# Kernel tuning notes

Measured on AMD Instinct MI355X. Metric: run time of the kernel, lower is better.

Reference implementation:

```python
import jax, jax.numpy as jnp
import numpy as np

B, N, M = 8, 1024, 64          # graphs, ops/graph, machines/graph
OPF, MF = 16, 8                # raw feature dims
H, D, L = 8, 64, 3             # heads, head dim, HGT layers
F = H * D                      # 512 = hidden_dim * num_heads
KC = 8                         # compatible machines per op
NOP, NM = B * N, B * M
EPS = 1e-5


def _graph_ln(x, w, b):
    # PyG LayerNorm(mode='graph') with batch=None: scalar mean/std over the whole tensor
    x = x - x.mean()
    return x / (x.std() + EPS) * w + b


def _seg_softmax(a, idx, n):
    amax = jax.ops.segment_max(a, idx, num_segments=n)
    amax = jnp.where(jnp.isfinite(amax), amax, 0.0)
    ex = jnp.exp(a - amax[idx])
    s = jax.ops.segment_sum(ex, idx, num_segments=n)
    return ex / (s[idx] + 1e-16)


def _forward(op_x, machine_x, W_emb_op, b_emb_op, W_emb_m, b_emb_m,
             opn_w, opn_b, mn_w, mn_b, Wk, bk, Wq, bq, Wv, bv,
             A_rel, M_rel, p_rel, W_out, b_out, skip, ln_w, ln_b,
             ei_precedes, ei_canproc, ei_compat):
    x_op = _graph_ln(op_x @ W_emb_op + b_emb_op, opn_w, opn_b)
    x_m = _graph_ln(machine_x @ W_emb_m + b_emb_m, mn_w, mn_b)
    s0, d0 = ei_precedes   # op -> op
    s1, d1 = ei_canproc    # machine -> op
    s2, d2 = ei_compat     # op -> machine
    scale = 1.0 / jnp.sqrt(jnp.float32(D))
    for l in range(L):
        k_op = (x_op @ Wk[l, 0] + bk[l, 0]).reshape(NOP, H, D)
        q_op = (x_op @ Wq[l, 0] + bq[l, 0]).reshape(NOP, H, D)
        v_op = (x_op @ Wv[l, 0] + bv[l, 0]).reshape(NOP, H, D)
        k_m = (x_m @ Wk[l, 1] + bk[l, 1]).reshape(NM, H, D)
        q_m = (x_m @ Wq[l, 1] + bq[l, 1]).reshape(NM, H, D)
        v_m = (x_m @ Wv[l, 1] + bv[l, 1]).reshape(NM, H, D)
        # relation-specific per-head transforms (a_rel/m_rel of HGTConv)
        k0 = jnp.einsum('nhd,hde->nhe', k_op, A_rel[l, 0]); v0 = jnp.einsum('nhd,hde->nhe', v_op, M_rel[l, 0])
        k1 = jnp.einsum('nhd,hde->nhe', k_m, A_rel[l, 1]);  v1 = jnp.einsum('nhd,hde->nhe', v_m, M_rel[l, 1])
        k2 = jnp.einsum('nhd,hde->nhe', k_op, A_rel[l, 2]); v2 = jnp.einsum('nhd,hde->nhe', v_op, M_rel[l, 2])
        # attention into op nodes: joint softmax over both incoming edge types
        a0 = (q_op[d0] * k0[s0]).sum(-1) * p_rel[l, 0] * scale   # [E0,H]
        a1 = (q_op[d1] * k1[s1]).sum(-1) * p_rel[l, 1] * scale   # [E1,H]
        a_op = jnp.concatenate([a0, a1]); dd = jnp.concatenate([d0, d1])
        w = _seg_softmax(a_op, dd, NOP)
        msg = jnp.concatenate([v0[s0], v1[s1]]) * w[:, :, None]
        agg_op = jax.ops.segment_sum(msg, dd, num_segments=NOP).reshape(NOP, F)
        # attention into machine nodes
        a2 = (q_m[d2] * k2[s2]).sum(-1) * p_rel[l, 2] * scale
        w2 = _seg_softmax(a2, d2, NM)
        agg_m = jax.ops.segment_sum(v2[s2] * w2[:, :, None], d2, num_segments=NM).reshape(NM, F)
        # output projection + learned skip gate (HGTConv internals)
        o_op = jax.nn.gelu(agg_op, approximate=False) @ W_out[l, 0] + b_out[l, 0]
        o_m = jax.nn.gelu(agg_m, approximate=False) @ W_out[l, 1] + b_out[l, 1]
        g_op = jax.nn.sigmoid(skip[l, 0]); g_m = jax.nn.sigmoid(skip[l, 1])
        o_op = g_op * o_op + (1.0 - g_op) * x_op
        o_m = g_m * o_m + (1.0 - g_m) * x_m
        # wrapper residual + dropout(eval=identity) + graph layer norm
        x_op = _graph_ln(o_op + x_op, ln_w[l], ln_b[l])
        x_m = _graph_ln(o_m + x_m, ln_w[l], ln_b[l])
    fea_j = x_op.reshape(B, N, F)
    fea_m = x_m.reshape(B, M, F)
    return fea_j, fea_m, fea_j.mean(1, keepdims=True), fea_m.mean(1, keepdims=True)


def setup_inputs() -> dict:
    key = jax.random.key(0)
    ks = jax.random.split(key, 12)
    rng = np.random.default_rng(0)
    ids = np.arange(NOP).reshape(B, N)
    src0 = ids[:, :-1].ravel(); dst0 = ids[:, 1:].ravel()
    mach = rng.integers(0, M, size=(B, N, KC)) + (np.arange(B) * M)[:, None, None]
    ops = np.broadcast_to(ids[:, :, None], (B, N, KC))
    ei_precedes = jnp.asarray(np.stack([src0, dst0]), dtype=jnp.int32)
    ei_canproc = jnp.asarray(np.stack([mach.ravel(), ops.ravel()]), dtype=jnp.int32)
    ei_compat = jnp.asarray(np.stack([ops.ravel(), mach.ravel()]), dtype=jnp.int32)
    n = lambda k, sh, s=0.05: jax.random.normal(k, sh, dtype=jnp.float32) * s
    return dict(
        op_x=n(ks[0], (NOP, OPF), 1.0),
        machine_x=n(ks[1], (NM, MF), 1.0),
        W_emb_op=n(ks[2], (OPF, F)), b_emb_op=jnp.zeros((F,), jnp.float32),
        W_emb_m=n(ks[3], (MF, F)), b_emb_m=jnp.zeros((F,), jnp.float32),
        opn_w=jnp.ones((F,), jnp.float32), opn_b=jnp.zeros((F,), jnp.float32),
        mn_w=jnp.ones((F,), jnp.float32), mn_b=jnp.zeros((F,), jnp.float32),
        Wk=n(ks[4], (L, 2, F, F)), bk=jnp.zeros((L, 2, F), jnp.float32),
        Wq=n(ks[5], (L, 2, F, F)), bq=jnp.zeros((L, 2, F), jnp.float32),
        Wv=n(ks[6], (L, 2, F, F)), bv=jnp.zeros((L, 2, F), jnp.float32),
        A_rel=n(ks[7], (L, 3, H, D, D)), M_rel=n(ks[8], (L, 3, H, D, D)),
        p_rel=jnp.ones((L, 3, H), jnp.float32),
        W_out=n(ks[9], (L, 2, F, F)), b_out=jnp.zeros((L, 2, F), jnp.float32),
        skip=jnp.ones((L, 2), jnp.float32),
        ln_w=jnp.ones((L, F), jnp.float32), ln_b=jnp.zeros((L, F), jnp.float32),
        ei_precedes=ei_precedes, ei_canproc=ei_canproc, ei_compat=ei_compat,
    )


def reference(op_x, machine_x, W_emb_op, b_emb_op, W_emb_m, b_emb_m,
              opn_w, opn_b, mn_w, mn_b, Wk, bk, Wq, bq, Wv, bv,
              A_rel, M_rel, p_rel, W_out, b_out, skip, ln_w, ln_b,
              ei_precedes, ei_canproc, ei_compat):
    return _forward(op_x, machine_x, W_emb_op, b_emb_op, W_emb_m, b_emb_m,
                    opn_w, opn_b, mn_w, mn_b, Wk, bk, Wq, bq, Wv, bv,
                    A_rel, M_rel, p_rel, W_out, b_out, skip, ln_w, ln_b,
                    ei_precedes, ei_canproc, ei_compat)
```

## Files before the change

kernel.cpp:

```cpp
#include <hip/hip_runtime.h>

typedef unsigned short u16;
typedef __attribute__((ext_vector_type(4))) float floatx4;
typedef __attribute__((ext_vector_type(8))) short shortx8;
typedef __attribute__((ext_vector_type(4))) short shortx4;

#define NOPS 8192
#define NMS  512
#define CQ   2560
#define CM   1536
#define NE2  65536
#define TOPC (NOPS*512)
#define TMC  (NMS*512)

__device__ __forceinline__ float bf2f(u16 u){ return __uint_as_float(((unsigned)u)<<16); }
__device__ __forceinline__ u16 f2bf(float f){
  unsigned u = __float_as_uint(f);
  u += 0x7FFFu + ((u>>16)&1u);
  return (u16)(u>>16);
}
__device__ __forceinline__ float wred(float v){
  #pragma unroll
  for (int o=32;o;o>>=1) v += __shfl_xor(v,o,64);
  return v;
}
__device__ __forceinline__ float wredmax(float v){
  #pragma unroll
  for (int o=32;o;o>>=1) v = fmaxf(v, __shfl_xor(v,o,64));
  return v;
}
__device__ __forceinline__ float geluf(float x){
  return 0.5f*x*(1.f+erff(x*0.70710678118654752f));
}
__device__ __forceinline__ void block_stat_out2(float s, float s2, float* pstat, int slot){
  __shared__ float sb[8];
  s = wred(s); s2 = wred(s2);
  int wv = threadIdx.x >> 6;
  if ((threadIdx.x & 63) == 0){ sb[wv*2] = s; sb[wv*2+1] = s2; }
  __syncthreads();
  if (threadIdx.x == 0){
    float a = 0.f, b = 0.f;
    int nw = blockDim.x >> 6;
    for (int i=0;i<nw;++i){ a += sb[i*2]; b += sb[i*2+1]; }
    pstat[slot*2]   = a;
    pstat[slot*2+1] = b;
  }
}

__global__ __launch_bounds__(256) void cnt2_k(const int* __restrict__ s1, float* __restrict__ Ct,
                                              float* __restrict__ Cn){
  int idx = blockIdx.x*256 + threadIdx.x;
  int n = idx >> 6, l = idx & 63;
  const int* row = s1 + n*8;
  int cnt = 0;
  #pragma unroll
  for (int j=0;j<8;++j) cnt += ((row[j] & 63) == l);
  float f = (float)cnt;
  Cn[(size_t)n*64 + l] = f;
  int b = n >> 10, nl = n & 1023;
  Ct[(size_t)((b<<6) + l)*1024 + nl] = f;
}

__global__ __launch_bounds__(256) void twout_k(const float* __restrict__ src, u16* __restrict__ dst){
  __shared__ u16 t[64][65];
  int l = blockIdx.x, kb = blockIdx.y*64, nb = blockIdx.z*64;
  const float* s = src + (size_t)l*262144;
  u16* d = dst + (size_t)l*262144;
  int tx = threadIdx.x & 63, ty4 = threadIdx.x >> 6;
  #pragma unroll 4
  for (int p=0;p<16;++p){
    int k = ty4 + p*4;
    t[k][tx] = f2bf(s[(size_t)(kb+k)*512 + nb + tx]);
  }
  __syncthreads();
  #pragma unroll 4
  for (int p=0;p<16;++p){
    int n = ty4 + p*4;
    d[(size_t)(nb+n)*512 + kb + tx] = t[tx][n];
  }
}

__global__ __launch_bounds__(256) void tq_k(const float* __restrict__ Wq,
                                            u16* __restrict__ Wc_op_t, u16* __restrict__ Wc_m_t){
  __shared__ u16 tl[64][65];
  int blk = blockIdx.x;
  int l = blk >> 1, side = blk & 1;
  const float* s = Wq + (size_t)blk*262144;
  u16* d = side ? (Wc_m_t + (size_t)l*CM*512) : (Wc_op_t + (size_t)l*CQ*512);
  int kb = blockIdx.y*64, nb = blockIdx.z*64;
  int tx = threadIdx.x & 63, ty4 = threadIdx.x >> 6;
  #pragma unroll 4
  for (int p=0;p<16;++p){
    int k = ty4 + p*4;
    tl[k][tx] = f2bf(s[(size_t)(kb+k)*512 + nb + tx]);
  }
  __syncthreads();
  #pragma unroll 4
  for (int p=0;p<16;++p){
    int n = ty4 + p*4;
    d[(size_t)(nb+n)*512 + kb + tx] = tl[tx][n];
  }
}

__global__ void qb_k(const float* __restrict__ bq, float* bias_op, float* bias_m){
  int i = blockIdx.x*blockDim.x + threadIdx.x;
  if (i >= 3072) return;
  int l = i >> 10, side = (i >> 9) & 1, f = i & 511;
  float v = bq[(l*2+side)*512 + f];
  if (side==0) bias_op[l*CQ + f] = v; else bias_m[l*CM + f] = v;
}

__global__ __launch_bounds__(256) void combine3_k(const float* __restrict__ Wk, const float* __restrict__ Wv,
                                                  const float* __restrict__ Ar, const float* __restrict__ Mr,
                                                  u16* __restrict__ Wc_op_t, u16* __restrict__ Wc_m_t){
  __shared__ u16 As[64*72];
  __shared__ u16 Bs[128*72];
  int gx = blockIdx.x;
  int l = gx/48; int rem = gx - l*48; int s = rem >> 3; int h = rem & 7;
  int side = (s < 4) ? 0 : 1;
  int r = (s < 4) ? (s+1) : (s-3);
  int useK = side==0 ? (s==0 || s==2) : (s==4);
  int rel  = side==0 ? ((s<2)?0:2) : 1;
  const float* W   = (useK ? Wk : Wv) + (size_t)(l*2+side)*262144;
  const float* Rel = (useK ? Ar : Mr) + ((size_t)(l*3+rel)*8 + h)*4096;
  int h64 = h*64;
  u16* Wt = side ? (Wc_m_t + (size_t)l*CM*512) : (Wc_op_t + (size_t)l*CQ*512);
  int rbase = r*512 + h64;
  int cc0 = blockIdx.y * 128;
  int tid = threadIdx.x, lane = tid & 63, wave = tid >> 6;
  {
    int d = tid >> 2, e0 = (tid & 3) * 16;
    #pragma unroll
    for (int j=0;j<16;++j) As[(e0+j)*72 + d] = f2bf(Rel[d*64 + e0 + j]);
  }
  {
    int ccl = tid >> 1, d0 = (tid & 1) * 32;
    const float* src = W + (size_t)(cc0+ccl)*512 + h64 + d0;
    #pragma unroll
    for (int j=0;j<32;j+=4){
      floatx4 v = *(const floatx4*)(src + j);
      shortx4 sv;
      #pragma unroll
      for (int e=0;e<4;++e) sv[e] = (short)f2bf(v[e]);
      *(shortx4*)(Bs + ccl*72 + d0 + j) = sv;
    }
  }
  __syncthreads();
  int wm = wave & 1, wn = wave >> 1;
  int mrow = lane & 15, quad = lane >> 4;
  floatx4 acc[2][4];
  #pragma unroll
  for (int a=0;a<2;++a)
    #pragma unroll
    for (int b=0;b<4;++b) acc[a][b] = (floatx4){0.f,0.f,0.f,0.f};
  #pragma unroll
  for (int ks=0; ks<2; ++ks){
    shortx8 af[2], bf[4];
    #pragma unroll
    for (int mt=0;mt<2;++mt) af[mt] = *(const shortx8*)(As + (wm*32 + mt*16 + mrow)*72 + ks*32 + quad*8);
    #pragma unroll
    for (int nt=0;nt<4;++nt) bf[nt] = *(const shortx8*)(Bs + (wn*64 + nt*16 + mrow)*72 + ks*32 + quad*8);
    #pragma unroll
    for (int mt=0;mt<2;++mt)
      #pragma unroll
      for (int nt=0;nt<4;++nt)
        acc[mt][nt] = __builtin_amdgcn_mfma_f32_16x16x32_bf16(af[mt], bf[nt], acc[mt][nt], 0, 0, 0);
  }
  #pragma unroll
  for (int mt=0;mt<2;++mt){
    #pragma unroll
    for (int nt=0;nt<4;++nt){
      int ccl = wn*64 + nt*16 + mrow;
      #pragma unroll
      for (int r2=0;r2<4;++r2){
        int e = wm*32 + mt*16 + quad*4 + r2;
        Wt[(size_t)(rbase + e)*512 + cc0 + ccl] = f2bf(acc[mt][nt][r2]);
      }
    }
  }
}
__global__ void cbias_k(const float* __restrict__ bk, const float* __restrict__ bv,
                        const float* __restrict__ Ar, const float* __restrict__ Mr,
                        float* bias_op, float* bias_m){
  int gx = blockIdx.x; int e = threadIdx.x;
  int l = gx/48; int rem = gx - l*48; int s = rem >> 3; int h = rem & 7;
  int side = (s < 4) ? 0 : 1;
  int r = (s < 4) ? (s+1) : (s-3);
  int useK = side==0 ? (s==0 || s==2) : (s==4);
  int rel  = side==0 ? ((s<2)?0:2) : 1;
  const float* bb  = (useK ? bk : bv) + (size_t)(l*2+side)*512 + h*64;
  const float* Rel = (useK ? Ar : Mr) + ((size_t)(l*3+rel)*8 + h)*4096;
  float acc = 0.f;
  for (int d=0; d<64; ++d) acc += bb[d]*Rel[d*64 + e];
  float* bias = side ? (bias_m + l*CM) : (bias_op + l*CQ);
  bias[r*512 + h*64 + e] = acc;
}

__global__ __launch_bounds__(256) void embed2_k(const float* __restrict__ Xop, const float* __restrict__ Wop,
                                                const float* __restrict__ bop, float* __restrict__ Yop,
                                                const float* __restrict__ Xm, const float* __restrict__ Wm,
                                                const float* __restrict__ bm_, float* __restrict__ Ym,
                                                float* pstat, float* pstat_m){
  int bid = blockIdx.x;
  const float *X, *W, *bias; float *Y, *ps; int K, total, nb, lb;
  if (bid < 1024){ X=Xop; W=Wop; bias=bop; Y=Yop; ps=pstat;   K=16; total=TOPC; nb=1024; lb=bid; }
  else           { X=Xm;  W=Wm;  bias=bm_; Y=Ym;  ps=pstat_m; K=8;  total=TMC;  nb=128;  lb=bid-1024; }
  float s = 0.f, s2 = 0.f;
  for (int idx = lb*256 + threadIdx.x; idx < total; idx += nb*256){
    int n = idx >> 9, f = idx & 511;
    float v = bias[f];
    for (int c=0;c<K;++c) v += X[n*K+c] * W[c*512+f];
    Y[idx] = v;
    s += v; s2 += v*v;
  }
  block_stat_out2(s, s2, ps, lb);
}

__global__ __launch_bounds__(256) void ln2_k(const float* __restrict__ src_op, float* __restrict__ dst_op,
                                             u16* __restrict__ dbf_op, const float* __restrict__ w_op,
                                             const float* __restrict__ b_op,
                                             const float* __restrict__ src_m, float* __restrict__ dst_m,
                                             u16* __restrict__ dbf_m, const float* __restrict__ w_m,
                                             const float* __restrict__ b_m,
                                             const float* __restrict__ pstat, const float* __restrict__ pstat_m,
                                             int nbo, int nbm){
  int bid = blockIdx.x;
  const float *src, *w, *b, *ps; float* dst; u16* dbf; int total4, nb, lb, nblk; float inv_n;
  if (bid < 1024){ src=src_op; dst=dst_op; dbf=dbf_op; w=w_op; b=b_op; ps=pstat;
                   total4=TOPC/4; nb=1024; lb=bid; nblk=nbo; inv_n=1.f/TOPC; }
  else           { src=src_m;  dst=dst_m;  dbf=dbf_m;  w=w_m;  b=b_m;  ps=pstat_m;
                   total4=TMC/4;  nb=128;  lb=bid-1024; nblk=nbm; inv_n=1.f/TMC; }
  __shared__ float sb[8];
  __shared__ float mr[2];
  float s = 0.f, s2 = 0.f;
  for (int i = threadIdx.x; i < nblk; i += 256){ s += ps[2*i]; s2 += ps[2*i+1]; }
  s = wred(s); s2 = wred(s2);
  int wv = threadIdx.x >> 6;
  if ((threadIdx.x & 63) == 0){ sb[wv*2] = s; sb[wv*2+1] = s2; }
  __syncthreads();
  if (threadIdx.x == 0){
    float a = 0.f, bsum = 0.f;
    for (int i=0;i<4;++i){ a += sb[i*2]; bsum += sb[i*2+1]; }
    float mean = a * inv_n;
    float var  = fmaxf(bsum * inv_n - mean*mean, 0.f);
    mr[0] = mean;
    mr[1] = 1.f/(sqrtf(var) + 1e-5f);
  }
  __syncthreads();
  float mean = mr[0], rinv = mr[1];
  const floatx4* s4 = (const floatx4*)src;
  floatx4* d4 = (floatx4*)dst;
  shortx4* db4 = (shortx4*)dbf;
  const floatx4* w4 = (const floatx4*)w;
  const floatx4* b4 = (const floatx4*)b;
  for (int i = lb*256 + threadIdx.x; i < total4; i += nb*256){
    int f = i & 127;
    floatx4 v = s4[i], wv2 = w4[f], bv = b4[f];
    shortx4 sv;
    #pragma unroll
    for (int e=0;e<4;++e){ v[e] = (v[e]-mean)*rinv*wv2[e] + bv[e]; sv[e] = (short)f2bf(v[e]); }
    d4[i] = v;
    db4[i] = sv;
  }
}

__device__ __forceinline__ void gemm_gate_core(u16* As, u16* Bs, const u16* __restrict__ A,
                                               const u16* __restrict__ Bt,
                                               const float* __restrict__ xr, const float* __restrict__ bo,
                                               const float* __restrict__ sk, float* __restrict__ Y,
                                               float* pstat, int slot, int bx, int by){
  const int tid = threadIdx.x;
  const int lane = tid & 63, wave = tid >> 6;
  const int bm = by * 128, bn = bx * 128;
  const int wm = wave & 1, wn = wave >> 1;
  const int mrow = lane & 15, quad = lane >> 4;
  const u16* Ab = A + (size_t)bm*512;
  const u16* Bb = Bt + (size_t)bn*512;
  floatx4 acc[4][4];
  #pragma unroll
  for (int a=0;a<4;++a)
    #pragma unroll
    for (int b=0;b<4;++b) acc[a][b] = (floatx4){0.f,0.f,0.f,0.f};
  const int r0 = tid >> 2, c0 = (tid & 3) * 8;
  const int r1 = (tid+256) >> 2, c1 = ((tid+256) & 3) * 8;
  const int lds0 = wave*512;
  const int lds1 = wave*512 + 2048;
  for (int k0 = 0; k0 < 512; k0 += 32){
    __builtin_amdgcn_global_load_lds((const __attribute__((address_space(1))) void*)(Ab + (size_t)r0*512 + k0 + c0),
                                     (__attribute__((address_space(3))) void*)(As + lds0), 16, 0, 0);
    __builtin_amdgcn_global_load_lds((const __attribute__((address_space(1))) void*)(Ab + (size_t)r1*512 + k0 + c1),
                                     (__attribute__((address_space(3))) void*)(As + lds1), 16, 0, 0);
    __builtin_amdgcn_global_load_lds((const __attribute__((address_space(1))) void*)(Bb + (size_t)r0*512 + k0 + c0),
                                     (__attribute__((address_space(3))) void*)(Bs + lds0), 16, 0, 0);
    __builtin_amdgcn_global_load_lds((const __attribute__((address_space(1))) void*)(Bb + (size_t)r1*512 + k0 + c1),
                                     (__attribute__((address_space(3))) void*)(Bs + lds1), 16, 0, 0);
    __syncthreads();
    shortx8 af[4], bf[4];
    #pragma unroll
    for (int mt=0;mt<4;++mt) af[mt] = *(const shortx8*)(As + (wm*64 + mt*16 + mrow)*32 + quad*8);
    #pragma unroll
    for (int nt=0;nt<4;++nt) bf[nt] = *(const shortx8*)(Bs + (wn*64 + nt*16 + mrow)*32 + quad*8);
    #pragma unroll
    for (int mt=0;mt<4;++mt)
      #pragma unroll
      for (int nt=0;nt<4;++nt)
        acc[mt][nt] = __builtin_amdgcn_mfma_f32_16x16x32_bf16(af[mt], bf[nt], acc[mt][nt], 0, 0, 0);
    __syncthreads();
  }
  float g = 1.f/(1.f+expf(-(*sk)));
  float s = 0.f, s2 = 0.f;
  #pragma unroll
  for (int mt=0;mt<4;++mt){
    #pragma unroll
    for (int nt=0;nt<4;++nt){
      int col = bn + wn*64 + nt*16 + mrow;
      float bval = bo[col];
      #pragma unroll
      for (int r2=0;r2<4;++r2){
        int row = bm + wm*64 + mt*16 + quad*4 + r2;
        float v = acc[mt][nt][r2] + bval;
        float o = g*v + (2.f-g)*xr[(size_t)row*512 + col];
        Y[(size_t)row*512 + col] = o;
        s += o; s2 += o*o;
      }
    }
  }
  block_stat_out2(s, s2, pstat, slot);
}
__global__ __launch_bounds__(256) void gemmgate2_k(const u16* A1, const u16* B1, const float* x1,
                                                   const float* bo1, const float* sk1, float* Y1, float* ps1,
                                                   int nblk1,
                                                   const u16* A2, const u16* B2, const float* x2,
                                                   const float* bo2, const float* sk2, float* Y2, float* ps2){
  __shared__ u16 As[128*32];
  __shared__ u16 Bs[128*32];
  int id = blockIdx.x;
  if (id < nblk1) gemm_gate_core(As, Bs, A1, B1, x1, bo1, sk1, Y1, ps1, id, id % 4, id / 4);
  else { int j = id - nblk1; gemm_gate_core(As, Bs, A2, B2, x2, bo2, sk2, Y2, ps2, j, j % 4, j / 4); }
}

__device__ __forceinline__ void stage_half8(const u16* __restrict__ src, int kc, u16* region, int tid){
  int wave = tid >> 6;
  #pragma unroll
  for (int j=0;j<2;++j){
    int idx = j*512 + tid;
    int row = idx >> 2, qp2 = idx & 3;
    int qs = qp2 ^ (((row >> 3) & 1) << 1);
    __builtin_amdgcn_global_load_lds(
      (const __attribute__((address_space(1))) void*)(src + (size_t)row*512 + kc + qs*8),
      (__attribute__((address_space(3))) void*)(region + (j*512 + wave*64)*8),
      16, 0, 0);
  }
}

#define MFMA_QUAD(MH) do { \
  __builtin_amdgcn_s_barrier(); \
  asm volatile("s_waitcnt lgkmcnt(0)" ::: "memory"); \
  __builtin_amdgcn_sched_barrier(0); \
  __builtin_amdgcn_s_setprio(1); \
  _Pragma("unroll") \
  for (int mt=0;mt<4;++mt){ \
    _Pragma("unroll") \
    for (int nt=0;nt<4;++nt) \
      acc[(MH)*4+mt][nt] = __builtin_amdgcn_mfma_f32_16x16x32_bf16(af[mt], bf[nt], acc[(MH)*4+mt][nt], 0, 0, 0); \
  } \
  __builtin_amdgcn_s_setprio(0); \
} while(0)

__global__ __launch_bounds__(512, 2) void gemm8_k(
    const u16* __restrict__ A1, const u16* __restrict__ B1, const float* __restrict__ bias1,
    u16* __restrict__ C1, int N1, int nbx1, int nblk1,
    const u16* __restrict__ A2, const u16* __restrict__ B2, const float* __restrict__ bias2,
    u16* __restrict__ C2, int N2, int nbx2){
  extern __shared__ u16 lds[];
  int id = blockIdx.x;
  const u16 *A, *Bt; const float* bias; u16* C; int N, bx, by;
  if (id < nblk1){
    int xcd = id & 7, loc = id >> 3;
    int wg = xcd * (nblk1 >> 3) + loc;
    A=A1; Bt=B1; bias=bias1; C=C1; N=N1; bx=wg%nbx1; by=wg/nbx1;
  }
  else { int j=id-nblk1; A=A2; Bt=B2; bias=bias2; C=C2; N=N2; bx=j%nbx2; by=j/nbx2; }
  const int tid = threadIdx.x, lane = tid & 63, wave = tid >> 6;
  const int wm = wave & 1, wn = wave >> 1;
  const int mrow = lane & 15, quad = lane >> 4;
  const int qp = quad ^ ((mrow & 8) ? 2 : 0);
  const u16* Ab = A + (size_t)(by*256)*512;
  const u16* Bb = Bt + (size_t)(bx*256)*512;

  floatx4 acc[8][4];
  #pragma unroll
  for (int a=0;a<8;++a)
    #pragma unroll
    for (int b=0;b<4;++b) acc[a][b] = (floatx4){0.f,0.f,0.f,0.f};

  stage_half8(Ab, 0,  lds,          tid);
  stage_half8(Bb, 0,  lds + 16384,  tid);
  stage_half8(Ab, 32, lds + 8192,   tid);
  stage_half8(Bb, 32, lds + 24576,  tid);
  stage_half8(Ab, 64, lds + 32768,  tid);
  stage_half8(Bb, 64, lds + 49152,  tid);
  asm volatile("s_waitcnt vmcnt(8)" ::: "memory");
  __builtin_amdgcn_s_barrier();

  for (int t = 0; t < 8; ++t){
    const int s = t & 1;
    u16* Sbase = lds + s*32768;
    u16* Obase = lds + (s^1)*32768;
    const u16* a0 = Sbase + (wm*128 + mrow)*32 + qp*8;
    const u16* b0 = Sbase + 16384 + (wn*64 + mrow)*32 + qp*8;
    const int kc1 = ((t < 7) ? (t+1) : 7)*64 + 32;
    const int kc2 = ((t < 6) ? (t+2) : 7)*64;
    shortx8 af[4], bf[4];

    #pragma unroll
    for (int mt=0;mt<4;++mt) af[mt] = *(const shortx8*)(a0 + mt*512);
    #pragma unroll
    for (int nt=0;nt<4;++nt) bf[nt] = *(const shortx8*)(b0 + nt*512);
    stage_half8(Ab, kc1, Obase + 8192, tid);
    MFMA_QUAD(0);
    __builtin_amdgcn_s_barrier();

    #pragma unroll
    for (int mt=0;mt<4;++mt) af[mt] = *(const shortx8*)(a0 + 2048 + mt*512);
    stage_half8(Bb, kc1, Obase + 24576, tid);
    MFMA_QUAD(1);
    asm volatile("s_waitcnt vmcnt(8)" ::: "memory");
    __builtin_amdgcn_s_barrier();

    #pragma unroll
    for (int mt=0;mt<4;++mt) af[mt] = *(const shortx8*)(a0 + 8192 + mt*512);
    #pragma unroll
    for (int nt=0;nt<4;++nt) bf[nt] = *(const shortx8*)(b0 + 8192 + nt*512);
    stage_half8(Ab, kc2, Sbase, tid);
    MFMA_QUAD(0);
    __builtin_amdgcn_s_barrier();

    #pragma unroll
    for (int mt=0;mt<4;++mt) af[mt] = *(const shortx8*)(a0 + 8192 + 2048 + mt*512);
    stage_half8(Bb, kc2, Sbase + 16384, tid);
    MFMA_QUAD(1);
    asm volatile("s_waitcnt vmcnt(8)" ::: "memory");
    __builtin_amdgcn_s_barrier();
  }

  const int crow0 = by*256 + wm*128 + quad*4;
  const int ccol0 = bx*256 + wn*64 + mrow;
  float bv[4];
  #pragma unroll
  for (int nt=0;nt<4;++nt) bv[nt] = bias ? bias[ccol0 + nt*16] : 0.f;
  #pragma unroll
  for (int mh=0;mh<2;++mh){
    #pragma unroll
    for (int mt=0;mt<4;++mt){
      int row = crow0 + mh*64 + mt*16;
      #pragma unroll
      for (int nt=0;nt<4;++nt){
        int col = ccol0 + nt*16;
        #pragma unroll
        for (int r2=0;r2<4;++r2)
          C[(size_t)(row+r2)*N + col] = f2bf(acc[mh*4+mt][nt][r2] + bv[nt]);
      }
    }
  }
}

__global__ __launch_bounds__(256) void qk12_k(const u16* __restrict__ qkv_op, const u16* __restrict__ qkv_m,
                                              const float* __restrict__ prel, const float* __restrict__ Cn,
                                              u16* __restrict__ W1, float* __restrict__ wpre,
                                              float* __restrict__ linv, float* __restrict__ S2f){
  __shared__ __align__(16) char smem[36864];
  u16* As = (u16*)smem;
  u16* Bs = As + 128*72;
  float* Sbuf = (float*)smem;
  int bh = blockIdx.y; int b = bh >> 3, h = bh & 7;
  int n0 = blockIdx.x * 128;
  int tid = threadIdx.x, lane = tid & 63, wave = tid >> 6;
  int mrow = lane & 15, quad = lane >> 4;
  if (blockIdx.z == 0){
    int wm = wave & 1, wn = wave >> 1;
    float p1 = prel[8 + h] * 0.125f;
    {
      int row = tid >> 1, col = (tid & 1) * 32;
      const u16* src = qkv_op + (size_t)(b*1024 + n0 + row)*CQ + h*64 + col;
      #pragma unroll
      for (int e=0;e<4;++e) *(shortx8*)(As + row*72 + col + e*8) = *(const shortx8*)(src + e*8);
    }
    {
      int row = tid >> 2, col = (tid & 3) * 16;
      const u16* src = qkv_m + (size_t)(b*64 + row)*CM + 512 + h*64 + col;
      *(shortx8*)(Bs + row*72 + col)     = *(const shortx8*)(src);
      *(shortx8*)(Bs + row*72 + col + 8) = *(const shortx8*)(src + 8);
    }
    __syncthreads();
    floatx4 acc[4][2];
    #pragma unroll
    for (int a=0;a<4;++a){ acc[a][0] = (floatx4){0,0,0,0}; acc[a][1] = (floatx4){0,0,0,0}; }
    #pragma unroll
    for (int ks=0; ks<2; ++ks){
      shortx8 af[4], bf[2];
      #pragma unroll
      for (int mt=0;mt<4;++mt) af[mt] = *(const shortx8*)(As + (wm*64 + mt*16 + mrow)*72 + ks*32 + quad*8);
      #pragma unroll
      for (int nt=0;nt<2;++nt) bf[nt] = *(const shortx8*)(Bs + (wn*32 + nt*16 + mrow)*72 + ks*32 + quad*8);
      #pragma unroll
      for (int mt=0;mt<4;++mt)
        #pragma unroll
        for (int nt=0;nt<2;++nt)
          acc[mt][nt] = __builtin_amdgcn_mfma_f32_16x16x32_bf16(af[mt], bf[nt], acc[mt][nt], 0, 0, 0);
    }
    __syncthreads();
    #pragma unroll
    for (int mt=0;mt<4;++mt){
      #pragma unroll
      for (int nt=0;nt<2;++nt){
        int m = wn*32 + nt*16 + mrow;
        #pragma unroll
        for (int r2=0;r2<4;++r2){
          int nl = wm*64 + mt*16 + quad*4 + r2;
          Sbuf[nl*65 + m] = acc[mt][nt][r2] * p1;
        }
      }
    }
    __syncthreads();
    if (tid < 128){
      int n_g = b*1024 + n0 + tid;
      int nl  = n0 + tid;
      float sp = -1e30f;
      if (nl > 0){
        float p0 = prel[h] * 0.125f;
        const u16* qp = qkv_op + (size_t)n_g*CQ + h*64;
        const u16* kp = qkv_op + (size_t)(n_g-1)*CQ + 512 + h*64;
        float d = 0.f;
        #pragma unroll
        for (int j=0;j<8;++j){
          shortx8 qa = *(const shortx8*)(qp + j*8);
          shortx8 ka = *(const shortx8*)(kp + j*8);
          #pragma unroll
          for (int e=0;e<8;++e) d += bf2f((u16)qa[e])*bf2f((u16)ka[e]);
        }
        sp = d * p0;
      }
      const float* crow = Cn + (size_t)n_g*64;
      float mx = sp;
      #pragma unroll
      for (int m=0;m<64;++m){
        if (crow[m] > 0.f) mx = fmaxf(mx, Sbuf[tid*65 + m]);
      }
      float L = 0.f;
      u16* wrow = W1 + ((size_t)n_g*8 + h)*64;
      #pragma unroll
      for (int m0=0;m0<64;m0+=4){
        shortx4 pv;
        #pragma unroll
        for (int e=0;e<4;++e){
          float c = crow[m0+e];
          float w = (c > 0.f) ? c*expf(Sbuf[tid*65 + m0+e]-mx) : 0.f;
          L += w;
          pv[e] = (short)f2bf(w);
        }
        *(shortx4*)(wrow + m0) = pv;
      }
      float ep = (nl > 0) ? expf(sp - mx) : 0.f;
      L += ep;
      wpre[(size_t)n_g*8 + h] = ep;
      linv[(size_t)n_g*8 + h] = 1.f/(L + 1e-16f);
    }
  } else {
    float p2 = prel[16 + h] * 0.125f;
    {
      int row = tid >> 2, col = (tid & 3) * 16;
      const u16* src = qkv_m + (size_t)(b*64+row)*CM + h*64 + col;
      *(shortx8*)(As + row*72 + col)     = *(const shortx8*)(src);
      *(shortx8*)(As + row*72 + col + 8) = *(const shortx8*)(src + 8);
    }
    {
      int row = tid >> 1, col = (tid & 1) * 32;
      const u16* src = qkv_op + (size_t)(b*1024 + n0 + row)*CQ + 1536 + h*64 + col;
      #pragma unroll
      for (int e=0;e<4;++e) *(shortx8*)(Bs + row*72 + col + e*8) = *(const shortx8*)(src + e*8);
    }
    __syncthreads();
    floatx4 acc[4][2];
    #pragma unroll
    for (int a=0;a<4;++a){ acc[a][0] = (floatx4){0,0,0,0}; acc[a][1] = (floatx4){0,0,0,0}; }
    #pragma unroll
    for (int ks=0; ks<2; ++ks){
      shortx8 af[4], bf[2];
      #pragma unroll
      for (int mt=0;mt<4;++mt) af[mt] = *(const shortx8*)(As + (mt*16 + mrow)*72 + ks*32 + quad*8);
      #pragma unroll
      for (int nt=0;nt<2;++nt) bf[nt] = *(const shortx8*)(Bs + (wave*32 + nt*16 + mrow)*72 + ks*32 + quad*8);
      #pragma unroll
      for (int mt=0;mt<4;++mt)
        #pragma unroll
        for (int nt=0;nt<2;++nt)
          acc[mt][nt] = __builtin_amdgcn_mfma_f32_16x16x32_bf16(af[mt], bf[nt], acc[mt][nt], 0, 0, 0);
    }
    #pragma unroll
    for (int mt=0;mt<4;++mt){
      #pragma unroll
      for (int nt=0;nt<2;++nt){
        int n = n0 + wave*32 + nt*16 + mrow;
        #pragma unroll
        for (int r2=0;r2<4;++r2){
          int m = mt*16 + quad*4 + r2;
          S2f[((size_t)(b*64 + m)*8 + h)*1024 + n] = acc[mt][nt][r2] * p2;
        }
      }
    }
  }
}

__global__ __launch_bounds__(512) void msoftm_k(const float* __restrict__ S2f, const float* __restrict__ Ct,
                                                u16* __restrict__ W2){
  int m = blockIdx.x;
  int h = threadIdx.x >> 6, d = threadIdx.x & 63;
  const float* srow = S2f + ((size_t)m*8 + h)*1024;
  const float* crow = Ct + (size_t)m*1024;
  float s[16], c[16];
  #pragma unroll
  for (int it=0; it<16; ++it){ s[it] = srow[it*64 + d]; c[it] = crow[it*64 + d]; }
  float mx = -1e30f;
  #pragma unroll
  for (int it=0; it<16; ++it) if (c[it] > 0.f) mx = fmaxf(mx, s[it]);
  mx = wredmax(mx);
  float e[16], L = 0.f;
  #pragma unroll
  for (int it=0; it<16; ++it){
    e[it] = (c[it] > 0.f) ? c[it]*expf(s[it]-mx) : 0.f;
    L += e[it];
  }
  L = wred(L);
  float inv = 1.f/(L + 1e-16f);
  u16* wrow = W2 + ((size_t)m*8 + h)*1024;
  #pragma unroll
  for (int it=0; it<16; ++it) wrow[it*64 + d] = f2bf(e[it]*inv);
}

__global__ __launch_bounds__(256) void agg12_k(const u16* __restrict__ W1, const u16* __restrict__ qkv_op,
                                               const u16* __restrict__ qkv_m, const float* __restrict__ wpre,
                                               const float* __restrict__ linv, u16* __restrict__ agg_op,
                                               const u16* __restrict__ W2, u16* __restrict__ agg_m){
  __shared__ u16 As[128*72];
  __shared__ u16 Bs[64*72];
  int bid = blockIdx.x;
  int tid = threadIdx.x, lane = tid & 63, wave = tid >> 6;
  int wm = wave & 1, wn = wave >> 1;
  int mrow = lane & 15, quad = lane >> 4;
  if (bid < 512){
    int bh = bid >> 3; int b = bh >> 3, h = bh & 7;
    int n0 = (bid & 7) * 128;
    {
      int row = tid >> 1, col = (tid & 1) * 32;
      const u16* src = W1 + ((size_t)(b*1024 + n0 + row)*8 + h)*64 + col;
      #pragma unroll
      for (int e=0;e<4;++e) *(shortx8*)(As + row*72 + col + e*8) = *(const shortx8*)(src + e*8);
    }
    {
      int m = tid >> 2, dcol = (tid & 3) * 16;
      const u16* src = qkv_m + (size_t)(b*64 + m)*CM + 1024 + h*64 + dcol;
      shortx8 v0 = *(const shortx8*)(src);
      shortx8 v1 = *(const shortx8*)(src + 8);
      #pragma unroll
      for (int e=0;e<8;++e){ Bs[(dcol+e)*72 + m] = (u16)v0[e]; Bs[(dcol+8+e)*72 + m] = (u16)v1[e]; }
    }
    __syncthreads();
    floatx4 acc[4][2];
    #pragma unroll
    for (int a=0;a<4;++a){ acc[a][0] = (floatx4){0,0,0,0}; acc[a][1] = (floatx4){0,0,0,0}; }
    #pragma unroll
    for (int ks=0; ks<2; ++ks){
      shortx8 af[4], bf[2];
      #pragma unroll
      for (int mt=0;mt<4;++mt) af[mt] = *(const shortx8*)(As + (wm*64 + mt*16 + mrow)*72 + ks*32 + quad*8);
      #pragma unroll
      for (int nt=0;nt<2;++nt) bf[nt] = *(const shortx8*)(Bs + (wn*32 + nt*16 + mrow)*72 + ks*32 + quad*8);
      #pragma unroll
      for (int mt=0;mt<4;++mt)
        #pragma unroll
        for (int nt=0;nt<2;++nt)
          acc[mt][nt] = __builtin_amdgcn_mfma_f32_16x16x32_bf16(af[mt], bf[nt], acc[mt][nt], 0, 0, 0);
    }
    #pragma unroll
    for (int mt=0;mt<4;++mt){
      #pragma unroll
      for (int nt=0;nt<2;++nt){
        int d = wn*32 + nt*16 + mrow;
        #pragma unroll
        for (int r2=0;r2<4;++r2){
          int n = n0 + wm*64 + mt*16 + quad*4 + r2;
          size_t ng = (size_t)b*1024 + n;
          size_t ih = ng*8 + h;
          float v = acc[mt][nt][r2];
          if ((n & 1023) > 0) v += wpre[ih] * bf2f(qkv_op[(ng-1)*CQ + 1024 + h*64 + d]);
          v *= linv[ih];
          agg_op[ng*512 + h*64 + d] = f2bf(geluf(v));
        }
      }
    }
  } else {
    int bh = bid - 512; int b = bh >> 3, h = bh & 7;
    floatx4 acc[2][2];
    acc[0][0]=(floatx4){0,0,0,0}; acc[0][1]=(floatx4){0,0,0,0};
    acc[1][0]=(floatx4){0,0,0,0}; acc[1][1]=(floatx4){0,0,0,0};
    const int arow = tid >> 2, acol = (tid & 3) * 8;
    const int nrow = tid >> 3, dcol = (tid & 7) * 8;
    for (int ks = 0; ks < 32; ++ks){
      int nn0 = ks*32;
      *(shortx8*)(As + arow*40 + acol) =
          *(const shortx8*)(W2 + ((size_t)(b*64 + arow)*8 + h)*1024 + nn0 + acol);
      shortx8 vv = *(const shortx8*)(qkv_op + (size_t)(b*1024 + nn0 + nrow)*CQ + 2048 + h*64 + dcol);
      #pragma unroll
      for (int e=0;e<8;++e) Bs[(dcol+e)*40 + nrow] = (u16)vv[e];
      __syncthreads();
      shortx8 af[2], bf[2];
      #pragma unroll
      for (int mt=0;mt<2;++mt) af[mt] = *(const shortx8*)(As + (wm*32 + mt*16 + mrow)*40 + quad*8);
      #pragma unroll
      for (int nt=0;nt<2;++nt) bf[nt] = *(const shortx8*)(Bs + (wn*32 + nt*16 + mrow)*40 + quad*8);
      #pragma unroll
      for (int mt=0;mt<2;++mt)
        #pragma unroll
        for (int nt=0;nt<2;++nt)
          acc[mt][nt] = __builtin_amdgcn_mfma_f32_16x16x32_bf16(af[mt], bf[nt], acc[mt][nt], 0, 0, 0);
      __syncthreads();
    }
    #pragma unroll
    for (int mt=0;mt<2;++mt){
      #pragma unroll
      for (int nt=0;nt<2;++nt){
        int dd = wn*32 + nt*16 + mrow;
        #pragma unroll
        for (int r2=0;r2<4;++r2){
          int m = wm*32 + mt*16 + quad*4 + r2;
          agg_m[(size_t)(b*64 + m)*512 + h*64 + dd] = f2bf(geluf(acc[mt][nt][r2]));
        }
      }
    }
  }
}

__global__ __launch_bounds__(512) void meanj_part_k(const float* __restrict__ xo, float* scratchJ){
  int b = blockIdx.x, chunk = blockIdx.y, f = threadIdx.x;
  float s = 0.f;
  for (int r=0;r<128;++r){
    int row = b*1024 + chunk*128 + r;
    s += xo[(size_t)row*512 + f];
  }
  scratchJ[(b*8 + chunk)*512 + f] = s;
}
__global__ __launch_bounds__(512) void mean2_k(const float* __restrict__ scratchJ, float* __restrict__ out){
  int i = blockIdx.x*512 + threadIdx.x;
  if (i < 4096){
    int b = i >> 9, f = i & 511;
    float s = 0.f;
    #pragma unroll
    for (int c=0;c<8;++c) s += scratchJ[(b*8+c)*512 + f];
    out[4456448 + i] = s * (1.f/1024.f);
  } else {
    int j = i - 4096;
    int b = j >> 9, f = j & 511;
    float s = 0.f;
    for (int r=0;r<64;++r) s += out[(size_t)TOPC + (size_t)(b*64+r)*512 + f];
    out[4460544 + j] = s * (1.f/64.f);
  }
}

extern "C" void kernel_launch(void* const* d_in, const int* in_sizes, int n_in,
                              void* d_out, int out_size, void* d_ws, size_t ws_size,
                              hipStream_t stream){
  const float* op_x      = (const float*)d_in[0];
  const float* machine_x = (const float*)d_in[1];
  const float* W_emb_op  = (const float*)d_in[2];
  const float* b_emb_op  = (const float*)d_in[3];
  const float* W_emb_m   = (const float*)d_in[4];
  const float* b_emb_m   = (const float*)d_in[5];
  const float* opn_w     = (const float*)d_in[6];
  const float* opn_b     = (const float*)d_in[7];
  const float* mn_w      = (const float*)d_in[8];
  const float* mn_b      = (const float*)d_in[9];
  const float* Wk        = (const float*)d_in[10];
  const float* bk        = (const float*)d_in[11];
  const float* Wq        = (const float*)d_in[12];
  const float* bq        = (const float*)d_in[13];
  const float* Wv        = (const float*)d_in[14];
  const float* bv        = (const float*)d_in[15];
  const float* A_rel     = (const float*)d_in[16];
  const float* M_rel     = (const float*)d_in[17];
  const float* p_rel     = (const float*)d_in[18];
  const float* W_out     = (const float*)d_in[19];
  const float* b_out     = (const float*)d_in[20];
  const float* skip      = (const float*)d_in[21];
  const float* ln_w      = (const float*)d_in[22];
  const float* ln_b      = (const float*)d_in[23];
  const int* s1          = (const int*)d_in[25];
  float* out = (float*)d_out;

  char* ws = (char*)d_ws;
  size_t off = 0;
  auto alloc = [&](size_t bytes)->void*{
    void* p = ws + off;
    off = (off + bytes + 255) & ~(size_t)255;
    return p;
  };
  float* pstat     = (float*)alloc(4096*4);
  float* scratchJ  = (float*)alloc(32768*4);
  float* Ct        = (float*)alloc((size_t)NMS*1024*4);
  float* Cn        = (float*)alloc((size_t)NOPS*64*4);
  float* S2f       = (float*)alloc((size_t)NMS*8*1024*4);
  u16*   W2        = (u16*)  alloc((size_t)NMS*8*1024*2);
  u16*   W1        = (u16*)  alloc((size_t)NOPS*8*64*2);
  float* wpre      = (float*)alloc((size_t)NOPS*8*4);
  float* linv      = (float*)alloc((size_t)NOPS*8*4);
  float* x_op      = (float*)alloc((size_t)NOPS*512*4);
  u16*   x_op_bf   = (u16*)  alloc((size_t)NOPS*512*2);
  float* x_m       = (float*)alloc((size_t)NMS*512*4);
  u16*   x_m_bf    = (u16*)  alloc((size_t)NMS*512*2);
  u16*   qkv_op    = (u16*)  alloc((size_t)NOPS*CQ*2);
  u16*   qkv_m     = (u16*)  alloc((size_t)NMS*CM*2);
  u16*   agg_op    = (u16*)  alloc((size_t)NOPS*512*2);
  u16*   agg_m     = (u16*)  alloc((size_t)NMS*512*2);
  u16*   Wc_op_t   = (u16*)  alloc((size_t)3*CQ*512*2);
  float* bias_op   = (float*)alloc((size_t)3*CQ*4);
  u16*   Wc_m_t    = (u16*)  alloc((size_t)3*CM*512*2);
  float* bias_m    = (float*)alloc((size_t)3*CM*4);
  u16*   Wout_t    = (u16*)  alloc((size_t)6*262144*2);
  float* o_op      = (float*)qkv_op;
  float* o_m       = (float*)qkv_m;
  float* pstat_m   = pstat + 2048;

  cnt2_k<<<2048,256,0,stream>>>(s1, Ct, Cn);
  twout_k<<<dim3(6,8,8),256,0,stream>>>(W_out, Wout_t);
  tq_k<<<dim3(6,8,8),256,0,stream>>>(Wq, Wc_op_t, Wc_m_t);
  qb_k<<<12,256,0,stream>>>(bq, bias_op, bias_m);
  combine3_k<<<dim3(144,4),256,0,stream>>>(Wk, Wv, A_rel, M_rel, Wc_op_t, Wc_m_t);
  cbias_k<<<144,64,0,stream>>>(bk, bv, A_rel, M_rel, bias_op, bias_m);

  embed2_k<<<1152,256,0,stream>>>(op_x, W_emb_op, b_emb_op, x_op,
                                  machine_x, W_emb_m, b_emb_m, x_m, pstat, pstat_m);
  ln2_k<<<1152,256,0,stream>>>(x_op, x_op, x_op_bf, opn_w, opn_b,
                               x_m, x_m, x_m_bf, mn_w, mn_b, pstat, pstat_m, 1024, 128);

  for (int l=0; l<3; ++l){
    int last = (l == 2);
    gemm8_k<<<332,512,131072,stream>>>(x_op_bf, Wc_op_t + (size_t)l*CQ*512, bias_op + l*CQ, qkv_op, CQ, 10, 320,
                                       x_m_bf, Wc_m_t + (size_t)l*CM*512, bias_m + l*CM, qkv_m, CM, 6);
    qk12_k<<<dim3(8,64,2),256,0,stream>>>(qkv_op, qkv_m, p_rel + l*24, Cn, W1, wpre, linv, S2f);
    msoftm_k<<<NMS,512,0,stream>>>(S2f, Ct, W2);
    agg12_k<<<576,256,0,stream>>>(W1, qkv_op, qkv_m, wpre, linv, agg_op, W2, agg_m);
    gemmgate2_k<<<272,256,0,stream>>>(agg_op, Wout_t + (size_t)(l*2+0)*262144, x_op,
                                      b_out + (size_t)(l*2+0)*512, skip + l*2+0, o_op, pstat, 256,
                                      agg_m, Wout_t + (size_t)(l*2+1)*262144, x_m,
                                      b_out + (size_t)(l*2+1)*512, skip + l*2+1, o_m, pstat_m);
    ln2_k<<<1152,256,0,stream>>>(o_op, last ? out : x_op, x_op_bf, ln_w + l*512, ln_b + l*512,
                                 o_m, last ? (out + TOPC) : x_m, x_m_bf, ln_w + l*512, ln_b + l*512,
                                 pstat, pstat_m, 256, 16);
  }

  meanj_part_k<<<dim3(8,8),512,0,stream>>>(out, scratchJ);
  mean2_k<<<16,512,0,stream>>>(scratchJ, out);
}
```

Before: 615.5 us.

## Fuse op-side attention aggregation into qk12 kernel and merge weight transposes

The op-node attention aggregation (P·V1 MFMA plus the predecessor term, normalisation and GELU) now runs inside qk12_k. The softmax weights, pre-edge weight and inverse sum stay in shared memory instead of being written to global W1/wpre/linv and read back by a separate kernel. The machine-side aggregation becomes its own small kernel of 64 blocks, and the two weight transpose kernels merge into one launch. This removes global round trips and launches, but qk12_k now needs 64KB of LDS, which may lower occupancy.

```diff
diff --git a/kernel.cpp b/kernel.cpp
--- a/kernel.cpp
+++ b/kernel.cpp
@@ -61,11 +61,21 @@
   Ct[(size_t)((b<<6) + l)*1024 + nl] = f;
 }
 
-__global__ __launch_bounds__(256) void twout_k(const float* __restrict__ src, u16* __restrict__ dst){
+__global__ __launch_bounds__(256) void tw_k(const float* __restrict__ Wout, const float* __restrict__ Wq,
+                                            u16* __restrict__ Wout_t, u16* __restrict__ Wc_op_t,
+                                            u16* __restrict__ Wc_m_t){
   __shared__ u16 t[64][65];
-  int l = blockIdx.x, kb = blockIdx.y*64, nb = blockIdx.z*64;
-  const float* s = src + (size_t)l*262144;
-  u16* d = dst + (size_t)l*262144;
+  int g = blockIdx.x;
+  const float* s; u16* d;
+  if (g < 6){
+    s = Wout + (size_t)g*262144;
+    d = Wout_t + (size_t)g*262144;
+  } else {
+    int blk = g - 6; int l = blk >> 1, side = blk & 1;
+    s = Wq + (size_t)blk*262144;
+    d = side ? (Wc_m_t + (size_t)l*CM*512) : (Wc_op_t + (size_t)l*CQ*512);
+  }
+  int kb = blockIdx.y*64, nb = blockIdx.z*64;
   int tx = threadIdx.x & 63, ty4 = threadIdx.x >> 6;
   #pragma unroll 4
   for (int p=0;p<16;++p){
@@ -77,28 +87,6 @@
   for (int p=0;p<16;++p){
     int n = ty4 + p*4;
     d[(size_t)(nb+n)*512 + kb + tx] = t[tx][n];
-  }
-}
-
-__global__ __launch_bounds__(256) void tq_k(const float* __restrict__ Wq,
-                                            u16* __restrict__ Wc_op_t, u16* __restrict__ Wc_m_t){
-  __shared__ u16 tl[64][65];
-  int blk = blockIdx.x;
-  int l = blk >> 1, side = blk & 1;
-  const float* s = Wq + (size_t)blk*262144;
-  u16* d = side ? (Wc_m_t + (size_t)l*CM*512) : (Wc_op_t + (size_t)l*CQ*512);
-  int kb = blockIdx.y*64, nb = blockIdx.z*64;
-  int tx = threadIdx.x & 63, ty4 = threadIdx.x >> 6;
-  #pragma unroll 4
-  for (int p=0;p<16;++p){
-    int k = ty4 + p*4;
-    tl[k][tx] = f2bf(s[(size_t)(kb+k)*512 + nb + tx]);
-  }
-  __syncthreads();
-  #pragma unroll 4
-  for (int p=0;p<16;++p){
-    int n = ty4 + p*4;
-    d[(size_t)(nb+n)*512 + kb + tx] = tl[tx][n];
   }
 }
 
@@ -467,12 +455,15 @@
 
 __global__ __launch_bounds__(256) void qk12_k(const u16* __restrict__ qkv_op, const u16* __restrict__ qkv_m,
                                               const float* __restrict__ prel, const float* __restrict__ Cn,
-                                              u16* __restrict__ W1, float* __restrict__ wpre,
-                                              float* __restrict__ linv, float* __restrict__ S2f){
-  __shared__ __align__(16) char smem[36864];
+                                              float* __restrict__ S2f, u16* __restrict__ agg_op){
+  __shared__ __align__(16) char smem[65536];
   u16* As = (u16*)smem;
   u16* Bs = As + 128*72;
   float* Sbuf = (float*)smem;
+  u16* P     = (u16*)(smem + 36864);
+  u16* v1T   = (u16*)(smem + 55296);
+  float* linvS = (float*)(smem + 64512);
+  float* wpreS = (float*)(smem + 65024);
   int bh = blockIdx.y; int b = bh >> 3, h = bh & 7;
   int n0 = blockIdx.x * 128;
   int tid = threadIdx.x, lane = tid & 63, wave = tid >> 6;
@@ -491,6 +482,14 @@
       const u16* src = qkv_m + (size_t)(b*64 + row)*CM + 512 + h*64 + col;
       *(shortx8*)(Bs + row*72 + col)     = *(const shortx8*)(src);
       *(shortx8*)(Bs + row*72 + col + 8) = *(const shortx8*)(src + 8);
+    }
+    {
+      int m = tid >> 2, dcol = (tid & 3) * 16;
+      const u16* src = qkv_m + (size_t)(b*64 + m)*CM + 1024 + h*64 + dcol;
+      shortx8 v0 = *(const shortx8*)(src);
+      shortx8 v1 = *(const shortx8*)(src + 8);
+      #pragma unroll
+      for (int e=0;e<8;++e){ v1T[(dcol+e)*72 + m] = (u16)v0[e]; v1T[(dcol+8+e)*72 + m] = (u16)v1[e]; }
     }
     __syncthreads();
     floatx4 acc[4][2];
@@ -548,7 +547,7 @@
         if (crow[m] > 0.f) mx = fmaxf(mx, Sbuf[tid*65 + m]);
       }
       float L = 0.f;
-      u16* wrow = W1 + ((size_t)n_g*8 + h)*64;
+      u16* prow = P + tid*72;
       #pragma unroll
       for (int m0=0;m0<64;m0+=4){
         shortx4 pv;
@@ -559,12 +558,46 @@
           L += w;
           pv[e] = (short)f2bf(w);
         }
-        *(shortx4*)(wrow + m0) = pv;
+        *(shortx4*)(prow + m0) = pv;
       }
       float ep = (nl > 0) ? expf(sp - mx) : 0.f;
       L += ep;
-      wpre[(size_t)n_g*8 + h] = ep;
-      linv[(size_t)n_g*8 + h] = 1.f/(L + 1e-16f);
+      wpreS[tid] = ep;
+      linvS[tid] = 1.f/(L + 1e-16f);
+    }
+    __syncthreads();
+    floatx4 po[4][2];
+    #pragma unroll
+    for (int a=0;a<4;++a){ po[a][0] = (floatx4){0,0,0,0}; po[a][1] = (floatx4){0,0,0,0}; }
+    #pragma unroll
+    for (int ks=0; ks<2; ++ks){
+      shortx8 paf[4], pbf[2];
+      #pragma unroll
+      for (int mt=0;mt<4;++mt) paf[mt] = *(const shortx8*)(P + (wm*64 + mt*16 + mrow)*72 + ks*32 + quad*8);
+      #pragma unroll
+      for (int nt=0;nt<2;++nt) pbf[nt] = *(const shortx8*)(v1T + (wn*32 + nt*16 + mrow)*72 + ks*32 + quad*8);
+      #pragma unroll
+      for (int mt=0;mt<4;++mt)
+        #pragma unroll
+        for (int nt=0;nt<2;++nt)
+          po[mt][nt] = __builtin_amdgcn_mfma_f32_16x16x32_bf16(paf[mt], pbf[nt], po[mt][nt], 0, 0, 0);
+    }
+    #pragma unroll
+    for (int mt=0;mt<4;++mt){
+      #pragma unroll
+      for (int nt=0;nt<2;++nt){
+        int d = wn*32 + nt*16 + mrow;
+        #pragma unroll
+        for (int r2=0;r2<4;++r2){
+          int rl = wm*64 + mt*16 + quad*4 + r2;
+          int n = n0 + rl;
+          size_t ng = (size_t)b*1024 + n;
+          float v = po[mt][nt][r2];
+          if (n > 0) v += wpreS[rl] * bf2f(qkv_op[(ng-1)*CQ + 1024 + h*64 + d]);
+          v *= linvS[rl];
+          agg_op[ng*512 + h*64 + d] = f2bf(geluf(v));
+        }
+      }
     }
   } else {
     float p2 = prel[16 + h] * 0.125f;
@@ -638,104 +671,48 @@
   for (int it=0; it<16; ++it) wrow[it*64 + d] = f2bf(e[it]*inv);
 }
 
-__global__ __launch_bounds__(256) void agg12_k(const u16* __restrict__ W1, const u16* __restrict__ qkv_op,
-                                               const u16* __restrict__ qkv_m, const float* __restrict__ wpre,
-                                               const float* __restrict__ linv, u16* __restrict__ agg_op,
-                                               const u16* __restrict__ W2, u16* __restrict__ agg_m){
-  __shared__ u16 As[128*72];
-  __shared__ u16 Bs[64*72];
-  int bid = blockIdx.x;
+__global__ __launch_bounds__(256) void aggm_k(const u16* __restrict__ qkv_op, const u16* __restrict__ W2,
+                                              u16* __restrict__ agg_m){
+  __shared__ u16 As[64*40];
+  __shared__ u16 Bs[64*40];
+  int bh = blockIdx.x; int b = bh >> 3, h = bh & 7;
   int tid = threadIdx.x, lane = tid & 63, wave = tid >> 6;
   int wm = wave & 1, wn = wave >> 1;
   int mrow = lane & 15, quad = lane >> 4;
-  if (bid < 512){
-    int bh = bid >> 3; int b = bh >> 3, h = bh & 7;
-    int n0 = (bid & 7) * 128;
-    {
-      int row = tid >> 1, col = (tid & 1) * 32;
-      const u16* src = W1 + ((size_t)(b*1024 + n0 + row)*8 + h)*64 + col;
-      #pragma unroll
-      for (int e=0;e<4;++e) *(shortx8*)(As + row*72 + col + e*8) = *(const shortx8*)(src + e*8);
-    }
-    {
-      int m = tid >> 2, dcol = (tid & 3) * 16;
-      const u16* src = qkv_m + (size_t)(b*64 + m)*CM + 1024 + h*64 + dcol;
-      shortx8 v0 = *(const shortx8*)(src);
-      shortx8 v1 = *(const shortx8*)(src + 8);
-      #pragma unroll
-      for (int e=0;e<8;++e){ Bs[(dcol+e)*72 + m] = (u16)v0[e]; Bs[(dcol+8+e)*72 + m] = (u16)v1[e]; }
-    }
+  floatx4 acc[2][2];
+  acc[0][0]=(floatx4){0,0,0,0}; acc[0][1]=(floatx4){0,0,0,0};
+  acc[1][0]=(floatx4){0,0,0,0}; acc[1][1]=(floatx4){0,0,0,0};
+  const int arow = tid >> 2, acol = (tid & 3) * 8;
+  const int nrow = tid >> 3, dcol = (tid & 7) * 8;
+  for (int ks = 0; ks < 32; ++ks){
+    int nn0 = ks*32;
+    *(shortx8*)(As + arow*40 + acol) =
+        *(const shortx8*)(W2 + ((size_t)(b*64 + arow)*8 + h)*1024 + nn0 + acol);
+    shortx8 vv = *(const shortx8*)(qkv_op + (size_t)(b*1024 + nn0 + nrow)*CQ + 2048 + h*64 + dcol);
+    #pragma unroll
+    for (int e=0;e<8;++e) Bs[(dcol+e)*40 + nrow] = (u16)vv[e];
     __syncthreads();
-    floatx4 acc[4][2];
-    #pragma unroll
-    for (int a=0;a<4;++a){ acc[a][0] = (floatx4){0,0,0,0}; acc[a][1] = (floatx4){0,0,0,0}; }
-    #pragma unroll
-    for (int ks=0; ks<2; ++ks){
-      shortx8 af[4], bf[2];
-      #pragma unroll
-      for (int mt=0;mt<4;++mt) af[mt] = *(const shortx8*)(As + (wm*64 + mt*16 + mrow)*72 + ks*32 + quad*8);
-      #pragma unroll
-      for (int nt=0;nt<2;++nt) bf[nt] = *(const shortx8*)(Bs + (wn*32 + nt*16 + mrow)*72 + ks*32 + quad*8);
-      #pragma unroll
-      for (int mt=0;mt<4;++mt)
-        #pragma unroll
-        for (int nt=0;nt<2;++nt)
-          acc[mt][nt] = __builtin_amdgcn_mfma_f32_16x16x32_bf16(af[mt], bf[nt], acc[mt][nt], 0, 0, 0);
-    }
-    #pragma unroll
-    for (int mt=0;mt<4;++mt){
-      #pragma unroll
-      for (int nt=0;nt<2;++nt){
-        int d = wn*32 + nt*16 + mrow;
-        #pragma unroll
-        for (int r2=0;r2<4;++r2){
-          int n = n0 + wm*64 + mt*16 + quad*4 + r2;
-          size_t ng = (size_t)b*1024 + n;
-          size_t ih = ng*8 + h;
-          float v = acc[mt][nt][r2];
-          if ((n & 1023) > 0) v += wpre[ih] * bf2f(qkv_op[(ng-1)*CQ + 1024 + h*64 + d]);
-          v *= linv[ih];
-          agg_op[ng*512 + h*64 + d] = f2bf(geluf(v));
-        }
-      }
-    }
-  } else {
-    int bh = bid - 512; int b = bh >> 3, h = bh & 7;
-    floatx4 acc[2][2];
-    acc[0][0]=(floatx4){0,0,0,0}; acc[0][1]=(floatx4){0,0,0,0};
-    acc[1][0]=(floatx4){0,0,0,0}; acc[1][1]=(floatx4){0,0,0,0};
-    const int arow = tid >> 2, acol = (tid & 3) * 8;
-    const int nrow = tid >> 3, dcol = (tid & 7) * 8;
-    for (int ks = 0; ks < 32; ++ks){
-      int nn0 = ks*32;
-      *(shortx8*)(As + arow*40 + acol) =
-          *(const shortx8*)(W2 + ((size_t)(b*64 + arow)*8 + h)*1024 + nn0 + acol);
-      shortx8 vv = *(const shortx8*)(qkv_op + (size_t)(b*1024 + nn0 + nrow)*CQ + 2048 + h*64 + dcol);
-      #pragma unroll
-      for (int e=0;e<8;++e) Bs[(dcol+e)*40 + nrow] = (u16)vv[e];
-      __syncthreads();
-      shortx8 af[2], bf[2];
-      #pragma unroll
-      for (int mt=0;mt<2;++mt) af[mt] = *(const shortx8*)(As + (wm*32 + mt*16 + mrow)*40 + quad*8);
-      #pragma unroll
-      for (int nt=0;nt<2;++nt) bf[nt] = *(const shortx8*)(Bs + (wn*32 + nt*16 + mrow)*40 + quad*8);
-      #pragma unroll
-      for (int mt=0;mt<2;++mt)
-        #pragma unroll
-        for (int nt=0;nt<2;++nt)
-          acc[mt][nt] = __builtin_amdgcn_mfma_f32_16x16x32_bf16(af[mt], bf[nt], acc[mt][nt], 0, 0, 0);
-      __syncthreads();
-    }
-    #pragma unroll
-    for (int mt=0;mt<2;++mt){
-      #pragma unroll
-      for (int nt=0;nt<2;++nt){
-        int dd = wn*32 + nt*16 + mrow;
-        #pragma unroll
-        for (int r2=0;r2<4;++r2){
-          int m = wm*32 + mt*16 + quad*4 + r2;
-          agg_m[(size_t)(b*64 + m)*512 + h*64 + dd] = f2bf(geluf(acc[mt][nt][r2]));
-        }
+    shortx8 af[2], bf[2];
+    #pragma unroll
+    for (int mt=0;mt<2;++mt) af[mt] = *(const shortx8*)(As + (wm*32 + mt*16 + mrow)*40 + quad*8);
+    #pragma unroll
+    for (int nt=0;nt<2;++nt) bf[nt] = *(const shortx8*)(Bs + (wn*32 + nt*16 + mrow)*40 + quad*8);
+    #pragma unroll
+    for (int mt=0;mt<2;++mt)
+      #pragma unroll
+      for (int nt=0;nt<2;++nt)
+        acc[mt][nt] = __builtin_amdgcn_mfma_f32_16x16x32_bf16(af[mt], bf[nt], acc[mt][nt], 0, 0, 0);
+    __syncthreads();
+  }
+  #pragma unroll
+  for (int mt=0;mt<2;++mt){
+    #pragma unroll
+    for (int nt=0;nt<2;++nt){
+      int dd = wn*32 + nt*16 + mrow;
+      #pragma unroll
+      for (int r2=0;r2<4;++r2){
+        int m = wm*32 + mt*16 + quad*4 + r2;
+        agg_m[(size_t)(b*64 + m)*512 + h*64 + dd] = f2bf(geluf(acc[mt][nt][r2]));
       }
     }
   }
@@ -810,9 +787,6 @@
   float* Cn        = (float*)alloc((size_t)NOPS*64*4);
   float* S2f       = (float*)alloc((size_t)NMS*8*1024*4);
   u16*   W2        = (u16*)  alloc((size_t)NMS*8*1024*2);
-  u16*   W1        = (u16*)  alloc((size_t)NOPS*8*64*2);
-  float* wpre      = (float*)alloc((size_t)NOPS*8*4);
-  float* linv      = (float*)alloc((size_t)NOPS*8*4);
   float* x_op      = (float*)alloc((size_t)NOPS*512*4);
   u16*   x_op_bf   = (u16*)  alloc((size_t)NOPS*512*2);
   float* x_m       = (float*)alloc((size_t)NMS*512*4);
@@ -831,8 +805,7 @@
   float* pstat_m   = pstat + 2048;
 
   cnt2_k<<<2048,256,0,stream>>>(s1, Ct, Cn);
-  twout_k<<<dim3(6,8,8),256,0,stream>>>(W_out, Wout_t);
-  tq_k<<<dim3(6,8,8),256,0,stream>>>(Wq, Wc_op_t, Wc_m_t);
+  tw_k<<<dim3(12,8,8),256,0,stream>>>(W_out, Wq, Wout_t, Wc_op_t, Wc_m_t);
   qb_k<<<12,256,0,stream>>>(bq, bias_op, bias_m);
   combine3_k<<<dim3(144,4),256,0,stream>>>(Wk, Wv, A_rel, M_rel, Wc_op_t, Wc_m_t);
   cbias_k<<<144,64,0,stream>>>(bk, bv, A_rel, M_rel, bias_op, bias_m);
@@ -846,9 +819,9 @@
     int last = (l == 2);
     gemm8_k<<<332,512,131072,stream>>>(x_op_bf, Wc_op_t + (size_t)l*CQ*512, bias_op + l*CQ, qkv_op, CQ, 10, 320,
                                        x_m_bf, Wc_m_t + (size_t)l*CM*512, bias_m + l*CM, qkv_m, CM, 6);
-    qk12_k<<<dim3(8,64,2),256,0,stream>>>(qkv_op, qkv_m, p_rel + l*24, Cn, W1, wpre, linv, S2f);
+    qk12_k<<<dim3(8,64,2),256,0,stream>>>(qkv_op, qkv_m, p_rel + l*24, Cn, S2f, agg_op);
     msoftm_k<<<NMS,512,0,stream>>>(S2f, Ct, W2);
-    agg12_k<<<576,256,0,stream>>>(W1, qkv_op, qkv_m, wpre, linv, agg_op, W2, agg_m);
+    aggm_k<<<64,256,0,stream>>>(qkv_op, W2, agg_m);
     gemmgate2_k<<<272,256,0,stream>>>(agg_op, Wout_t + (size_t)(l*2+0)*262144, x_op,
                                       b_out + (size_t)(l*2+0)*512, skip + l*2+0, o_op, pstat, 256,
                                       agg_m, Wout_t + (size_t)(l*2+1)*262144, x_m,
```

Result: slower. 630.7 us (+2.5%).
